# Performance work log

Measured on AMD Instinct MI355X. Metric: run time of the kernel, lower is better.

The kernel has to match this reference:

```python
import jax, jax.numpy as jnp
import numpy as np

LN_EPS = 1e-5  # torch LayerNorm default


def layer_norm(x, g, b):
    mu = jnp.mean(x, axis=-1, keepdims=True)
    var = jnp.mean((x - mu) ** 2, axis=-1, keepdims=True)
    return (x - mu) / jnp.sqrt(var + LN_EPS) * g + b


def setup_inputs() -> dict:
    key = jax.random.key(0)
    k0, k1 = jax.random.split(key, 2)
    B, C, N, T, D = 64, 2, 1024, 13, 256  # batch, in_dim, nodes, time_step+1, dim
    x = jax.random.normal(k0, (B, C, N, T), dtype=jnp.float32)
    conv_w = jax.random.normal(k1, (D, C, T), dtype=jnp.float32) * 0.05  # Conv2d kernel (1,T) squeezed
    conv_b = jnp.zeros((D,), dtype=jnp.float32)
    time_g = jnp.ones((D,), dtype=jnp.float32)
    time_b = jnp.zeros((D,), dtype=jnp.float32)
    static_g = jnp.ones((N,), dtype=jnp.float32)
    static_b = jnp.zeros((N,), dtype=jnp.float32)
    return {"x": x, "conv_w": conv_w, "conv_b": conv_b,
            "time_g": time_g, "time_b": time_b,
            "static_g": static_g, "static_b": static_b}


def reference(x, conv_w, conv_b, time_g, time_b, static_g, static_b):
    # Conv2d(in_dim, dim, kernel=(1, T)) on [B,C,N,T] -> [B,dim,N,1]; squeeze+transpose -> [B,N,dim]
    emb = jnp.einsum('bcnt,dct->bnd', x, conv_w) + conv_b
    emb = layer_norm(emb, time_g, time_b)  # [B, N, D]
    # Spearman rank correlation, batched (replaces Python loop over B)
    ranks = jnp.argsort(jnp.argsort(emb, axis=-1), axis=-1).astype(emb.dtype)  # [B,N,D]
    c = ranks - jnp.mean(ranks, axis=-1, keepdims=True)
    norm = jnp.sqrt(jnp.sum(c * c, axis=-1, keepdims=True))  # [B,N,1]
    corr = jnp.einsum('bnd,bmd->bnm', c, c)  # [B,N,N]
    adj = jnp.abs(corr / (norm * jnp.swapaxes(norm, -1, -2) + 1e-8))
    # LayerNorm over last (nodes) axis then ReLU
    return jax.nn.relu(layer_norm(adj, static_g, static_b))
```

## Files before the change

kernel.cpp:

```cpp
#include <hip/hip_runtime.h>


typedef __attribute__((ext_vector_type(4))) int i32x4;

__device__ __forceinline__ void load_lds16(const void* g, void* l) {
  __builtin_amdgcn_global_load_lds(
      (const __attribute__((address_space(1))) void*)g,
      (__attribute__((address_space(3))) void*)l, 16, 0, 0);
}

__global__ __launch_bounds__(256) void conv_rank_kernel(
    const float* __restrict__ x, const float* __restrict__ w,
    const float* __restrict__ cb, const float* __restrict__ tg,
    const float* __restrict__ tb, signed char* __restrict__ ranks)
{
  int row = blockIdx.x;
  int b = row >> 10, n = row & 1023;
  int d = threadIdx.x;
  int wave = d >> 6, lane = d & 63;

  __shared__ float xs[26];
  __shared__ float red[8];
  __shared__ unsigned int ks[256];

  if (d < 26) {
    int c = d / 13, t = d - c * 13;
    xs[d] = x[((size_t)(b * 2 + c) * 1024 + n) * 13 + t];
  }
  __syncthreads();

  const float* wd = w + d * 26;
  float acc = cb[d];
  #pragma unroll
  for (int i = 0; i < 26; ++i) acc += wd[i] * xs[i];

  float v1 = acc, v2 = acc * acc;
  #pragma unroll
  for (int o = 32; o > 0; o >>= 1) {
    v1 += __shfl_down(v1, o);
    v2 += __shfl_down(v2, o);
  }
  if (lane == 0) { red[wave * 2] = v1; red[wave * 2 + 1] = v2; }
  __syncthreads();
  float s1 = red[0] + red[2] + red[4] + red[6];
  float s2 = red[1] + red[3] + red[5] + red[7];
  float mu = s1 * (1.0f / 256.0f);
  float var = s2 * (1.0f / 256.0f) - mu * mu;
  float rs = rsqrtf(var + 1e-5f);
  float val = (acc - mu) * rs * tg[d] + tb[d];

  unsigned int u = __float_as_uint(val);
  unsigned int key = (u & 0x80000000u) ? ~u : (u | 0x80000000u);
  unsigned int okey = key;

  #pragma unroll
  for (int k = 2; k <= 256; k <<= 1) {
    #pragma unroll
    for (int j = k >> 1; j > 0; j >>= 1) {
      unsigned int pkey;
      if (j < 64) {
        pkey = __shfl_xor(key, j);
      } else {
        ks[d] = key;
        __syncthreads();
        pkey = ks[d ^ j];
        __syncthreads();
      }
      bool keep_min = ((d & j) == 0) == ((d & k) == 0);
      unsigned int mn = key < pkey ? key : pkey;
      unsigned int mx = key < pkey ? pkey : key;
      key = keep_min ? mn : mx;
    }
  }

  ks[d] = key;
  __syncthreads();
  int pos = 0;
  #pragma unroll
  for (int s = 128; s > 0; s >>= 1)
    pos += (ks[pos + s - 1] < okey) ? s : 0;

  ranks[(size_t)row * 256 + d] = (signed char)(pos - 128);
}

__global__ __launch_bounds__(512, 4) void corr_ln_kernel(
    const signed char* __restrict__ ranks, const float* __restrict__ sg,
    const float* __restrict__ sb, float* __restrict__ out)
{
  int bid = blockIdx.x;
  int blk = (bid & 7) * 256 + (bid >> 3);
  int b  = blk >> 5;
  int n0 = (blk & 31) << 5;
  const signed char* R = ranks + (size_t)b * 1024 * 256;
  float* O = out + ((size_t)b * 1024 + n0) * 1024;

  __shared__ __align__(16) signed char As[8192];
  __shared__ __align__(16) signed char Bs[65536];
  __shared__ float red[8][64];
  __shared__ float stats[2][32];

  int tid = threadIdx.x;
  int wave = tid >> 6, lane = tid & 63;
  int fr = lane & 15, quad = lane >> 4;
  int cw = wave << 7;

  {
    int o = tid * 16;
    int kt_a = o >> 11, kq = (o >> 9) & 3, r32 = (o >> 4) & 31;
    load_lds16(R + (size_t)(n0 + r32) * 256 + kt_a * 64 + kq * 16, As + o);
  }

  i32x4 acc[2][8] = {};

  for (int kt = 0; kt < 4; ++kt) {
    #pragma unroll
    for (int i = 0; i < 8; ++i) {
      int o = i * 8192 + tid * 16;
      int kq = o >> 14, row = (o & 16383) >> 4;
      load_lds16(R + (size_t)row * 256 + kt * 64 + kq * 16, Bs + o);
    }
    __syncthreads();

    i32x4 af0 = *(const i32x4*)(As + kt * 2048 + quad * 512 + fr * 16);
    i32x4 af1 = *(const i32x4*)(As + kt * 2048 + quad * 512 + (16 + fr) * 16);
    #pragma unroll
    for (int ni = 0; ni < 8; ++ni) {
      i32x4 bf = *(const i32x4*)(Bs + quad * 16384 + (cw + ni * 16 + fr) * 16);
      acc[0][ni] = __builtin_amdgcn_mfma_i32_16x16x64_i8(af0, bf, acc[0][ni], 0, 0, 0);
      acc[1][ni] = __builtin_amdgcn_mfma_i32_16x16x64_i8(af1, bf, acc[1][ni], 0, 0, 0);
    }
    __syncthreads();
  }

  float nrm = sqrtf(1398080.0f);
  float inv_den = 1.0f / (nrm * nrm + 1e-8f);

  float s[2][4], q[2][4];
  #pragma unroll
  for (int mi = 0; mi < 2; ++mi) {
    #pragma unroll
    for (int v = 0; v < 4; ++v) {
      float ss = 0.0f, qq = 0.0f;
      #pragma unroll
      for (int ni = 0; ni < 8; ++ni) {
        float a = fabsf((float)(acc[mi][ni][v] - 64)) * inv_den;
        ss += a; qq += a * a;
      }
      #pragma unroll
      for (int o = 8; o > 0; o >>= 1) {
        ss += __shfl_xor(ss, o);
        qq += __shfl_xor(qq, o);
      }
      s[mi][v] = ss; q[mi][v] = qq;
    }
  }
  if (fr == 0) {
    #pragma unroll
    for (int mi = 0; mi < 2; ++mi)
      #pragma unroll
      for (int v = 0; v < 4; ++v) {
        int r = mi * 16 + quad * 4 + v;
        red[wave][r] = s[mi][v];
        red[wave][32 + r] = q[mi][v];
      }
  }
  __syncthreads();

  if (tid < 32) {
    float su = 0.0f, sq = 0.0f;
    #pragma unroll
    for (int ww = 0; ww < 8; ++ww) { su += red[ww][tid]; sq += red[ww][32 + tid]; }
    float mu = su * (1.0f / 1024.0f);
    float var = sq * (1.0f / 1024.0f) - mu * mu;
    stats[0][tid] = mu;
    stats[1][tid] = rsqrtf(var + 1e-5f);
  }
  __syncthreads();

  float gv[8], bv[8];
  #pragma unroll
  for (int ni = 0; ni < 8; ++ni) {
    int col = cw + ni * 16 + fr;
    gv[ni] = sg[col];
    bv[ni] = sb[col];
  }
  #pragma unroll
  for (int mi = 0; mi < 2; ++mi) {
    #pragma unroll
    for (int v = 0; v < 4; ++v) {
      int r = mi * 16 + quad * 4 + v;
      float mu = stats[0][r], rs = stats[1][r];
      float* orow = O + (size_t)r * 1024;
      #pragma unroll
      for (int ni = 0; ni < 8; ++ni) {
        float a = fabsf((float)(acc[mi][ni][v] - 64)) * inv_den;
        orow[cw + ni * 16 + fr] = fmaxf(0.0f, (a - mu) * rs * gv[ni] + bv[ni]);
      }
    }
  }
}

extern "C" void kernel_launch(void* const* d_in, const int* in_sizes, int n_in,
                              void* d_out, int out_size, void* d_ws, size_t ws_size,
                              hipStream_t stream) {
  const float* x  = (const float*)d_in[0];
  const float* w  = (const float*)d_in[1];
  const float* cb = (const float*)d_in[2];
  const float* tg = (const float*)d_in[3];
  const float* tb = (const float*)d_in[4];
  const float* sg = (const float*)d_in[5];
  const float* sb = (const float*)d_in[6];
  float* out = (float*)d_out;
  signed char* ranks = (signed char*)d_ws;

  conv_rank_kernel<<<64 * 1024, 256, 0, stream>>>(x, w, cb, tg, tb, ranks);
  corr_ln_kernel<<<2048, 512, 0, stream>>>(ranks, sg, sb, out);
}
```

Before: 555.1 us.

## Process one row per wave in conv_rank kernel with register bitonic sort

The conv+LayerNorm+rank kernel now gives each wave its own row, and each lane holds 4 of the 256 elements. The large-stride bitonic stages become in-register compare-swaps, which removes the block-wide barriers and LDS round trips from the sort. The LayerNorm reductions are now wave-only shuffles. The grid shrinks by 4x, and each thread does more work and uses more registers.

```diff
diff --git a/kernel.cpp b/kernel.cpp
--- a/kernel.cpp
+++ b/kernel.cpp
@@ -14,73 +14,105 @@
     const float* __restrict__ cb, const float* __restrict__ tg,
     const float* __restrict__ tb, signed char* __restrict__ ranks)
 {
-  int row = blockIdx.x;
-  int b = row >> 10, n = row & 1023;
-  int d = threadIdx.x;
-  int wave = d >> 6, lane = d & 63;
-
-  __shared__ float xs[26];
-  __shared__ float red[8];
-  __shared__ unsigned int ks[256];
-
-  if (d < 26) {
-    int c = d / 13, t = d - c * 13;
-    xs[d] = x[((size_t)(b * 2 + c) * 1024 + n) * 13 + t];
-  }
-  __syncthreads();
-
-  const float* wd = w + d * 26;
-  float acc = cb[d];
-  #pragma unroll
-  for (int i = 0; i < 26; ++i) acc += wd[i] * xs[i];
-
-  float v1 = acc, v2 = acc * acc;
-  #pragma unroll
-  for (int o = 32; o > 0; o >>= 1) {
-    v1 += __shfl_down(v1, o);
-    v2 += __shfl_down(v2, o);
-  }
-  if (lane == 0) { red[wave * 2] = v1; red[wave * 2 + 1] = v2; }
-  __syncthreads();
-  float s1 = red[0] + red[2] + red[4] + red[6];
-  float s2 = red[1] + red[3] + red[5] + red[7];
+  int grp = blockIdx.x;
+  int b = grp >> 8;
+  int n0 = (grp & 255) << 2;
+  int tid = threadIdx.x;
+  int wave = tid >> 6, lane = tid & 63;
+  int row = b * 1024 + n0 + wave;
+
+  __shared__ float xs[4][26];
+  __shared__ unsigned int ws[4][256];
+
+  if (tid < 104) {
+    int c = tid / 52, rem = tid - c * 52;
+    int r = rem / 13, t = rem - r * 13;
+    xs[r][c * 13 + t] = x[((size_t)(b * 2 + c) * 1024 + n0 + r) * 13 + t];
+  }
+  __syncthreads();
+
+  float accv[4];
+  #pragma unroll
+  for (int i = 0; i < 4; ++i) {
+    int d = i * 64 + lane;
+    const float2* wp = (const float2*)(w + d * 26);
+    float a = cb[d];
+    #pragma unroll
+    for (int u = 0; u < 13; ++u) {
+      float2 w2 = wp[u];
+      a += w2.x * xs[wave][2 * u] + w2.y * xs[wave][2 * u + 1];
+    }
+    accv[i] = a;
+  }
+
+  float s1 = accv[0] + accv[1] + accv[2] + accv[3];
+  float s2 = accv[0] * accv[0] + accv[1] * accv[1] +
+             accv[2] * accv[2] + accv[3] * accv[3];
+  #pragma unroll
+  for (int o = 1; o < 64; o <<= 1) {
+    s1 += __shfl_xor(s1, o);
+    s2 += __shfl_xor(s2, o);
+  }
   float mu = s1 * (1.0f / 256.0f);
   float var = s2 * (1.0f / 256.0f) - mu * mu;
   float rs = rsqrtf(var + 1e-5f);
-  float val = (acc - mu) * rs * tg[d] + tb[d];
-
-  unsigned int u = __float_as_uint(val);
-  unsigned int key = (u & 0x80000000u) ? ~u : (u | 0x80000000u);
-  unsigned int okey = key;
+
+  unsigned int key[4], okey[4];
+  #pragma unroll
+  for (int i = 0; i < 4; ++i) {
+    int d = i * 64 + lane;
+    float val = (accv[i] - mu) * rs * tg[d] + tb[d];
+    unsigned int u = __float_as_uint(val);
+    key[i] = (u & 0x80000000u) ? ~u : (u | 0x80000000u);
+    okey[i] = key[i];
+  }
 
   #pragma unroll
   for (int k = 2; k <= 256; k <<= 1) {
     #pragma unroll
     for (int j = k >> 1; j > 0; j >>= 1) {
-      unsigned int pkey;
       if (j < 64) {
-        pkey = __shfl_xor(key, j);
+        #pragma unroll
+        for (int i = 0; i < 4; ++i) {
+          unsigned int pk = __shfl_xor(key[i], j);
+          int e = i * 64 + lane;
+          bool km = ((e & j) == 0) == ((e & k) == 0);
+          unsigned int mn = key[i] < pk ? key[i] : pk;
+          unsigned int mx = key[i] < pk ? pk : key[i];
+          key[i] = km ? mn : mx;
+        }
       } else {
-        ks[d] = key;
-        __syncthreads();
-        pkey = ks[d ^ j];
-        __syncthreads();
-      }
-      bool keep_min = ((d & j) == 0) == ((d & k) == 0);
-      unsigned int mn = key < pkey ? key : pkey;
-      unsigned int mx = key < pkey ? pkey : key;
-      key = keep_min ? mn : mx;
-    }
-  }
-
-  ks[d] = key;
-  __syncthreads();
-  int pos = 0;
-  #pragma unroll
-  for (int s = 128; s > 0; s >>= 1)
-    pos += (ks[pos + s - 1] < okey) ? s : 0;
-
-  ranks[(size_t)row * 256 + d] = (signed char)(pos - 128);
+        int di = j >> 6;
+        #pragma unroll
+        for (int i = 0; i < 4; ++i) {
+          if ((i & di) == 0) {
+            int ip = i + di;
+            int e = i * 64 + lane;
+            bool up = ((e & k) == 0);
+            unsigned int a = key[i], bb = key[ip];
+            unsigned int mn = a < bb ? a : bb;
+            unsigned int mx = a < bb ? bb : a;
+            key[i]  = up ? mn : mx;
+            key[ip] = up ? mx : mn;
+          }
+        }
+      }
+    }
+  }
+
+  #pragma unroll
+  for (int i = 0; i < 4; ++i) ws[wave][i * 64 + lane] = key[i];
+  __syncthreads();
+  int pos[4] = {0, 0, 0, 0};
+  #pragma unroll
+  for (int s = 128; s > 0; s >>= 1) {
+    #pragma unroll
+    for (int i = 0; i < 4; ++i)
+      pos[i] += (ws[wave][pos[i] + s - 1] < okey[i]) ? s : 0;
+  }
+  #pragma unroll
+  for (int i = 0; i < 4; ++i)
+    ranks[(size_t)row * 256 + i * 64 + lane] = (signed char)(pos[i] - 128);
 }
 
 __global__ __launch_bounds__(512, 4) void corr_ln_kernel(
@@ -213,6 +245,6 @@
   float* out = (float*)d_out;
   signed char* ranks = (signed char*)d_ws;
 
-  conv_rank_kernel<<<64 * 1024, 256, 0, stream>>>(x, w, cb, tg, tb, ranks);
+  conv_rank_kernel<<<16384, 256, 0, stream>>>(x, w, cb, tg, tb, ranks);
   corr_ln_kernel<<<2048, 512, 0, stream>>>(ranks, sg, sb, out);
 }
```

Result: faster. 529.9 us (-4.5%).
